# Performance work log

Hardware: AMD Instinct MI355X
Metric: run time of the kernel (lower is better)

Reference implementation:

```python
import jax, jax.numpy as jnp
import numpy as np

B, T, D, H = 2, 2048, 2048, 16
HS = D // H  # head size 128


def setup_inputs() -> dict:
    key = jax.random.key(0)
    ks = jax.random.split(key, 5)
    s = 0.02
    return {
        "x": jax.random.normal(ks[0], (B, T, D), dtype=jnp.float32),
        "wq": jax.random.normal(ks[1], (D, D), dtype=jnp.float32) * s,
        "wk": jax.random.normal(ks[2], (D, D), dtype=jnp.float32) * s,
        "wv": jax.random.normal(ks[3], (D, D), dtype=jnp.float32) * s,
        "wo": jax.random.normal(ks[4], (D, D), dtype=jnp.float32) * s,
    }


def reference(x, wq, wk, wv, wo):
    b, t, d = x.shape
    # projections: nn.Linear(x) = x @ W.T ; here W stored as (out,in)
    q = (x @ wq.T).reshape(b, t, H, HS).transpose(0, 2, 1, 3)  # (B,H,T,HS)
    k = (x @ wk.T).reshape(b, t, H, HS).transpose(0, 2, 1, 3)
    v = (x @ wv.T).reshape(b, t, H, HS).transpose(0, 2, 1, 3)
    scale = 1.0 / np.sqrt(HS).astype(np.float32)
    e = jnp.einsum("bhqd,bhkd->bhqk", q, k) * scale  # (B,H,T,T)
    causal = jnp.tril(jnp.ones((t, t), dtype=bool))
    e = jnp.where(causal[None, None], e, jnp.float32(-jnp.inf))
    alpha = jax.nn.softmax(e, axis=-1)  # dropout=0.0 -> identity
    attn = jnp.einsum("bhqk,bhkd->bhqd", alpha, v)
    attn = attn.transpose(0, 2, 1, 3).reshape(b, t, d)
    return attn @ wo.T
```

## Files before the change

kernel.cpp:

```cpp
#include <hip/hip_runtime.h>
#include <hip/hip_bf16.h>

typedef __bf16 bf16x8 __attribute__((ext_vector_type(8)));
typedef float f32x4 __attribute__((ext_vector_type(4)));
typedef unsigned short u16x8 __attribute__((ext_vector_type(8)));

#define GLDS16(g, s)                                                         \
  __builtin_amdgcn_global_load_lds(                                          \
      (const __attribute__((address_space(1))) void*)(g),                    \
      (__attribute__((address_space(3))) void*)(s), 16, 0, 0)

__device__ __forceinline__ void store1(__hip_bfloat16* p, float v) { *p = __float2bfloat16(v); }
__device__ __forceinline__ void store1(float* p, float v) { *p = v; }

__global__ __launch_bounds__(256) void cast_f32_to_bf16(const float4* __restrict__ in,
                                                        ushort4* __restrict__ out, int n4) {
  int i = blockIdx.x * 256 + threadIdx.x;
  if (i >= n4) return;
  float4 v = in[i];
  union { ushort4 u; __hip_bfloat16 h[4]; } o;
  o.h[0] = __float2bfloat16(v.x);
  o.h[1] = __float2bfloat16(v.y);
  o.h[2] = __float2bfloat16(v.z);
  o.h[3] = __float2bfloat16(v.w);
  out[i] = o.u;
}

template <typename OutT>
__global__ __launch_bounds__(512, 2) void gemm256(const __hip_bfloat16* __restrict__ A,
                                                  const __hip_bfloat16* __restrict__ B0,
                                                  const __hip_bfloat16* __restrict__ B1,
                                                  const __hip_bfloat16* __restrict__ B2,
                                                  OutT* __restrict__ C0,
                                                  OutT* __restrict__ C1,
                                                  OutT* __restrict__ C2,
                                                  int nBx, int nBy, int ntPerMat,
                                                  int N, int K) {
  __shared__ __hip_bfloat16 As[2][256 * 64];
  __shared__ __hip_bfloat16 Bs[2][256 * 64];

  const int t = threadIdx.x;
  const int w = t >> 6, l = t & 63;
  const int lr = l & 15, hi = l >> 4;

  const int nwg = nBx * nBy;
  int id = (int)blockIdx.x;
  id = (id & 7) * (nwg >> 3) + (id >> 3);
  const int bx = id / nBy;
  const int by = id % nBy;

  const int sel = bx / ntPerMat;
  const __hip_bfloat16* Bm = (sel == 0) ? B0 : ((sel == 1) ? B1 : B2);
  OutT* Cm = (sel == 0) ? C0 : ((sel == 1) ? C1 : C2);
  const int n0 = (bx - sel * ntPerMat) * 256;
  const int m0 = by * 256;

  const int c0r = t >> 3, cs = t & 7;
  const int c1r = 64 + c0r;
  const __hip_bfloat16* aP0 = A + (size_t)(m0 + c0r) * K + (cs ^ (c0r & 7)) * 8;
  const __hip_bfloat16* aP1 = A + (size_t)(m0 + c1r) * K + (cs ^ (c1r & 7)) * 8;
  const __hip_bfloat16* bP0 = Bm + (size_t)(n0 + c0r) * K + (cs ^ (c0r & 7)) * 8;
  const __hip_bfloat16* bP1 = Bm + (size_t)(n0 + c1r) * K + (cs ^ (c1r & 7)) * 8;
  const size_t HK = (size_t)128 * K;

#define STAGE_S(sidx, nb, koff)                                              \
  do {                                                                       \
    if ((sidx) == 0) {                                                       \
      GLDS16(aP0 + (koff), (char*)As[nb] + t * 16);                          \
      GLDS16(aP1 + (koff), (char*)As[nb] + 8192 + t * 16);                   \
    } else if ((sidx) == 1) {                                                \
      GLDS16(bP0 + (koff), (char*)Bs[nb] + t * 16);                          \
      GLDS16(bP1 + (koff), (char*)Bs[nb] + 8192 + t * 16);                   \
    } else if ((sidx) == 2) {                                                \
      GLDS16(aP0 + HK + (koff), (char*)As[nb] + 16384 + t * 16);             \
      GLDS16(aP1 + HK + (koff), (char*)As[nb] + 24576 + t * 16);             \
    } else {                                                                 \
      GLDS16(bP0 + HK + (koff), (char*)Bs[nb] + 16384 + t * 16);             \
      GLDS16(bP1 + HK + (koff), (char*)Bs[nb] + 24576 + t * 16);             \
    }                                                                        \
  } while (0)

  f32x4 acc[2][2][4][2] = {};
  bf16x8 af[4][2];
  bf16x8 bqA[2][2], bqB[2][2];
  const int NT = K / 64;
  const int sw = lr & 7;
  const int arow = (w >> 2) * 64;
  const int brow = (w & 3) * 32;

#define LOAD_A(mh)                                                           \
  _Pragma("unroll") for (int mi = 0; mi < 4; ++mi)                           \
    _Pragma("unroll") for (int kk = 0; kk < 2; ++kk)                         \
      af[mi][kk] = *(const bf16x8*)((const char*)As[buf] +                   \
          ((mh) * 128 + arow + mi * 16 + lr) * 128 + (((kk * 4 + hi) ^ sw) << 4));
#define LOAD_B(dst, nh)                                                      \
  _Pragma("unroll") for (int ni = 0; ni < 2; ++ni)                           \
    _Pragma("unroll") for (int kk = 0; kk < 2; ++kk)                         \
      dst[ni][kk] = *(const bf16x8*)((const char*)Bs[buf] +                  \
          ((nh) * 128 + brow + ni * 16 + lr) * 128 + (((kk * 4 + hi) ^ sw) << 4));
#define MFMA_Q(mh, nh, bq)                                                   \
  do {                                                                       \
    __builtin_amdgcn_s_setprio(1);                                           \
    _Pragma("unroll") for (int mi = 0; mi < 4; ++mi)                         \
      _Pragma("unroll") for (int ni = 0; ni < 2; ++ni) {                     \
        acc[mh][nh][mi][ni] = __builtin_amdgcn_mfma_f32_16x16x32_bf16(       \
            af[mi][0], bq[ni][0], acc[mh][nh][mi][ni], 0, 0, 0);             \
        acc[mh][nh][mi][ni] = __builtin_amdgcn_mfma_f32_16x16x32_bf16(       \
            af[mi][1], bq[ni][1], acc[mh][nh][mi][ni], 0, 0, 0);             \
      }                                                                      \
    __builtin_amdgcn_s_setprio(0);                                           \
  } while (0)
#define WAITB(lastt)                                                         \
  do {                                                                       \
    if (lastt) asm volatile("s_waitcnt vmcnt(0)" ::: "memory");              \
    else       asm volatile("s_waitcnt vmcnt(4)" ::: "memory");              \
    __builtin_amdgcn_s_barrier();                                            \
  } while (0)

  STAGE_S(0, 0, 0);
  STAGE_S(1, 0, 0);
  STAGE_S(3, 0, 0);
  STAGE_S(2, 0, 0);

  for (int tt = 0; tt < NT; ++tt) {
    const int buf = tt & 1, nb = buf ^ 1;
    const bool stg = (tt + 1 < NT);
    const bool lastt = !stg;
    const size_t ko = (size_t)(tt + 1) * 64;

    WAITB(lastt);
    LOAD_A(0); LOAD_B(bqA, 0);
    if (stg) STAGE_S(0, nb, ko);
    MFMA_Q(0, 0, bqA);

    WAITB(lastt);
    LOAD_B(bqB, 1);
    if (stg) STAGE_S(1, nb, ko);
    MFMA_Q(0, 1, bqB);

    WAITB(lastt);
    LOAD_A(1);
    if (stg) STAGE_S(3, nb, ko);
    MFMA_Q(1, 1, bqB);

    WAITB(lastt);
    if (stg) STAGE_S(2, nb, ko);
    MFMA_Q(1, 0, bqA);
  }
#undef WAITB
#undef MFMA_Q
#undef LOAD_B
#undef LOAD_A
#undef STAGE_S

#pragma unroll
  for (int mh = 0; mh < 2; ++mh)
#pragma unroll
    for (int nh = 0; nh < 2; ++nh)
#pragma unroll
      for (int mi = 0; mi < 4; ++mi)
#pragma unroll
        for (int ni = 0; ni < 2; ++ni)
#pragma unroll
          for (int i = 0; i < 4; ++i) {
            size_t idx = (size_t)(m0 + mh * 128 + arow + mi * 16 + hi * 4 + i) * N +
                         (n0 + nh * 128 + brow + ni * 16 + lr);
            store1(&Cm[idx], acc[mh][nh][mi][ni][i]);
          }
}

__global__ __launch_bounds__(256, 2) void flash_attn(const __hip_bfloat16* __restrict__ Qg,
                                                     const __hip_bfloat16* __restrict__ Kg,
                                                     const __hip_bfloat16* __restrict__ Vg,
                                                     __hip_bfloat16* __restrict__ Og) {
  __shared__ __hip_bfloat16 Ks[2][64 * 128];
  __shared__ __hip_bfloat16 Vt[128 * 64];

  const int mblk = blockIdx.x;
  const int bh = mblk & 31;
  const int jj = mblk >> 5;
  const int qt = (jj < 8) ? (15 - jj) : (jj - 8);
  const int b = bh >> 4, h = bh & 15;
  const int q0 = qt * 128;
  const int t = threadIdx.x, w = t >> 6, l = t & 63;
  const int lr = l & 15, hi = l >> 4;
  const size_t base = ((size_t)b * 2048) * 2048 + (size_t)h * 128;
  const int nt = 2 * qt + 2;
  const float scale = 0.08838834764831843f;

  const int hi2 = (hi & 1) * 2;
  const int addrA = (((hi2) << 4) | lr) << 2;
  const int addrB = (((hi2 + 1) << 4) | lr) << 2;
  int addr_o[4];
#pragma unroll
  for (int i = 0; i < 4; ++i) addr_o[i] = ((l & 48) | (hi * 4 + i)) << 2;
  const bool hiHigh = (hi >> 1) != 0;

  bf16x8 qf[2][4];
#pragma unroll
  for (int g = 0; g < 2; ++g) {
    const __hip_bfloat16* qrow = Qg + base + (size_t)(q0 + w * 32 + g * 16 + lr) * 2048;
#pragma unroll
    for (int kk = 0; kk < 4; ++kk)
      qf[g][kk] = *(const bf16x8*)(qrow + kk * 32 + hi * 8);
  }

  f32x4 o_acc[2][8] = {};
  float m_run[2] = {-1e30f, -1e30f};
  float l_run[2] = {0.f, 0.f};

  const __hip_bfloat16* kptr[4];
#pragma unroll
  for (int i = 0; i < 4; ++i) {
    int c = i * 256 + t;
    int kr = c >> 4;
    int ke = ((c & 15) ^ (kr & 7)) * 8;
    kptr[i] = Kg + base + (size_t)kr * 2048 + ke;
  }
  const __hip_bfloat16* vptr[2];
#pragma unroll
  for (int it = 0; it < 2; ++it) {
    int kp = it * 16 + w * 4 + hi;
    vptr[it] = Vg + base + (size_t)(kp * 2) * 2048 + lr * 8;
  }

  u16x8 va[2], vb[2];
#pragma unroll
  for (int i = 0; i < 4; ++i)
    GLDS16(kptr[i], (char*)Ks[0] + (i * 256 + t) * 16);
#pragma unroll
  for (int it = 0; it < 2; ++it) {
    va[it] = *(const u16x8*)vptr[it];
    vb[it] = *(const u16x8*)(vptr[it] + 2048);
  }

  for (int kt = 0; kt < nt; ++kt) {
    const int cur = kt & 1;
    const int kb = kt * 64;
    __syncthreads();

#pragma unroll
    for (int it = 0; it < 2; ++it)
#pragma unroll
      for (int j2 = 0; j2 < 8; ++j2) {
        int d = lr * 8 + j2;
        int sw = (lr ^ j2) & 7;
        int off = d * 128 + (((it * 4 + w) ^ sw) << 4) + hi * 4;
        *(unsigned int*)((char*)Vt + off) =
            (unsigned int)va[it][j2] | ((unsigned int)vb[it][j2] << 16);
      }
    if (kt + 1 < nt) {
      const size_t adv = (size_t)(kb + 64) * 2048;
#pragma unroll
      for (int i = 0; i < 4; ++i)
        GLDS16(kptr[i] + adv, (char*)Ks[cur ^ 1] + (i * 256 + t) * 16);
#pragma unroll
      for (int it = 0; it < 2; ++it) {
        va[it] = *(const u16x8*)(vptr[it] + adv);
        vb[it] = *(const u16x8*)(vptr[it] + adv + 2048);
      }
    }
    asm volatile("s_waitcnt lgkmcnt(0)" ::: "memory");
    __builtin_amdgcn_s_barrier();

    if (!(kt == nt - 1 && w < 2)) {
      const char* ks = (const char*)Ks[cur];

      f32x4 st[2][4];
#pragma unroll
      for (int g = 0; g < 2; ++g)
#pragma unroll
        for (int nk = 0; nk < 4; ++nk) { f32x4 z = {}; st[g][nk] = z; }
#pragma unroll
      for (int nk = 0; nk < 4; ++nk)
#pragma unroll
        for (int kk = 0; kk < 4; ++kk) {
          bf16x8 kf = *(const bf16x8*)(ks + (nk * 16 + lr) * 256 +
                                       (((kk * 4 + hi) ^ (lr & 7)) << 4));
#pragma unroll
          for (int g = 0; g < 2; ++g)
            st[g][nk] = __builtin_amdgcn_mfma_f32_16x16x32_bf16(kf, qf[g][kk], st[g][nk], 0, 0, 0);
        }

      const bool maskt = (kt >= nt - 2);
#pragma unroll
      for (int g = 0; g < 2; ++g)
#pragma unroll
        for (int nk = 0; nk < 4; ++nk)
#pragma unroll
          for (int i = 0; i < 4; ++i) {
            float v = st[g][nk][i] * scale;
            if (maskt) {
              int ki = kb + nk * 16 + hi * 4 + i;
              int qi = q0 + w * 32 + g * 16 + lr;
              if (ki > qi) v = -1e30f;
            }
            st[g][nk][i] = v;
          }

      bf16x8 paf[2][2];
#pragma unroll
      for (int g = 0; g < 2; ++g) {
        float t0 = fmaxf(fmaxf(st[g][0][0], st[g][0][1]), fmaxf(st[g][0][2], st[g][0][3]));
        float t1 = fmaxf(fmaxf(st[g][1][0], st[g][1][1]), fmaxf(st[g][1][2], st[g][1][3]));
        float t2 = fmaxf(fmaxf(st[g][2][0], st[g][2][1]), fmaxf(st[g][2][2], st[g][2][3]));
        float t3 = fmaxf(fmaxf(st[g][3][0], st[g][3][1]), fmaxf(st[g][3][2], st[g][3][3]));
        float mx = fmaxf(fmaxf(t0, t1), fmaxf(t2, t3));
        mx = fmaxf(mx, __shfl_xor(mx, 16));
        mx = fmaxf(mx, __shfl_xor(mx, 32));

        if (!__all(mx - m_run[g] <= 8.0f)) {
          float mnew = fmaxf(m_run[g], mx);
          float rs = __expf(m_run[g] - mnew);
          m_run[g] = mnew;
          l_run[g] *= rs;
          int rsi = __float_as_int(rs);
#pragma unroll
          for (int i = 0; i < 4; ++i) {
            float rso = __int_as_float(__builtin_amdgcn_ds_bpermute(addr_o[i], rsi));
#pragma unroll
            for (int nc = 0; nc < 8; ++nc) o_acc[g][nc][i] *= rso;
          }
        }

#pragma unroll
        for (int nk = 0; nk < 4; ++nk)
#pragma unroll
          for (int i = 0; i < 4; ++i)
            st[g][nk][i] = __expf(st[g][nk][i] - m_run[g]);

        float s0 = (st[g][0][0] + st[g][0][1]) + (st[g][0][2] + st[g][0][3]);
        float s1 = (st[g][1][0] + st[g][1][1]) + (st[g][1][2] + st[g][1][3]);
        float s2 = (st[g][2][0] + st[g][2][1]) + (st[g][2][2] + st[g][2][3]);
        float s3 = (st[g][3][0] + st[g][3][1]) + (st[g][3][2] + st[g][3][3]);
        float sm = (s0 + s1) + (s2 + s3);
        sm += __shfl_xor(sm, 16);
        sm += __shfl_xor(sm, 32);
        l_run[g] += sm;

        unsigned pk[4][2];
#pragma unroll
        for (int nk = 0; nk < 4; ++nk) {
          asm("v_cvt_pk_bf16_f32 %0, %1, %2"
              : "=v"(pk[nk][0]) : "v"(st[g][nk][0]), "v"(st[g][nk][1]));
          asm("v_cvt_pk_bf16_f32 %0, %1, %2"
              : "=v"(pk[nk][1]) : "v"(st[g][nk][2]), "v"(st[g][nk][3]));
        }

#pragma unroll
        for (int kk = 0; kk < 2; ++kk) {
          unsigned au[4];
#pragma unroll
          for (int p = 0; p < 4; ++p) {
            int ad = (p < 2) ? addrA : addrB;
            int v0 = __builtin_amdgcn_ds_bpermute(ad, (int)pk[2 * kk][p & 1]);
            int v1 = __builtin_amdgcn_ds_bpermute(ad, (int)pk[2 * kk + 1][p & 1]);
            au[p] = hiHigh ? (unsigned)v1 : (unsigned)v0;
          }
          union { unsigned u[4]; bf16x8 v; } cv;
          cv.u[0] = au[0]; cv.u[1] = au[1]; cv.u[2] = au[2]; cv.u[3] = au[3];
          paf[g][kk] = cv.v;
        }
      }

#pragma unroll
      for (int kk = 0; kk < 2; ++kk)
#pragma unroll
        for (int nc = 0; nc < 8; ++nc) {
          int d = nc * 16 + lr;
          int sw = ((d >> 3) ^ d) & 7;
          bf16x8 vfr = *(const bf16x8*)((const char*)Vt + d * 128 +
                                        (((kk * 4 + hi) ^ sw) << 4));
#pragma unroll
          for (int g = 0; g < 2; ++g)
            o_acc[g][nc] = __builtin_amdgcn_mfma_f32_16x16x32_bf16(paf[g][kk], vfr, o_acc[g][nc], 0, 0, 0);
        }
    }
  }

#pragma unroll
  for (int g = 0; g < 2; ++g) {
    float lo[4];
#pragma unroll
    for (int i = 0; i < 4; ++i)
      lo[i] = __int_as_float(__builtin_amdgcn_ds_bpermute(addr_o[i], __float_as_int(l_run[g])));
#pragma unroll
    for (int nc = 0; nc < 8; ++nc)
#pragma unroll
      for (int i = 0; i < 4; ++i) {
        float val = o_acc[g][nc][i] / lo[i];
        Og[base + (size_t)(q0 + w * 32 + g * 16 + hi * 4 + i) * 2048 + nc * 16 + lr] =
            __float2bfloat16(val);
      }
  }
}

extern "C" void kernel_launch(void* const* d_in, const int* in_sizes, int n_in,
                              void* d_out, int out_size, void* d_ws, size_t ws_size,
                              hipStream_t stream) {
  const float* x  = (const float*)d_in[0];
  const float* wq = (const float*)d_in[1];
  const float* wk = (const float*)d_in[2];
  const float* wv = (const float*)d_in[3];
  const float* wo = (const float*)d_in[4];
  float* out = (float*)d_out;

  const int BT = 4096, D = 2048;
  const size_t ND = (size_t)D * D;
  const size_t NX = (size_t)BT * D;

  __hip_bfloat16* xb  = (__hip_bfloat16*)d_ws;
  __hip_bfloat16* wqb = xb + NX;
  __hip_bfloat16* wkb = wqb + ND;
  __hip_bfloat16* wvb = wkb + ND;
  __hip_bfloat16* wob = wvb + ND;
  __hip_bfloat16* Qb  = wob + ND;
  __hip_bfloat16* Kb  = Qb + NX;
  __hip_bfloat16* Vb  = Kb + NX;
  __hip_bfloat16* Ab  = Vb + NX;

  cast_f32_to_bf16<<<(int)(NX / 4 / 256), 256, 0, stream>>>((const float4*)x,  (ushort4*)xb,  (int)(NX / 4));
  cast_f32_to_bf16<<<(int)(ND / 4 / 256), 256, 0, stream>>>((const float4*)wq, (ushort4*)wqb, (int)(ND / 4));
  cast_f32_to_bf16<<<(int)(ND / 4 / 256), 256, 0, stream>>>((const float4*)wk, (ushort4*)wkb, (int)(ND / 4));
  cast_f32_to_bf16<<<(int)(ND / 4 / 256), 256, 0, stream>>>((const float4*)wv, (ushort4*)wvb, (int)(ND / 4));
  cast_f32_to_bf16<<<(int)(ND / 4 / 256), 256, 0, stream>>>((const float4*)wo, (ushort4*)wob, (int)(ND / 4));

  gemm256<__hip_bfloat16><<<384, 512, 0, stream>>>(xb, wqb, wkb, wvb, Qb, Kb, Vb,
                                                   24, 16, 8, D, D);

  flash_attn<<<512, 256, 0, stream>>>(Qb, Kb, Vb, Ab);

  gemm256<float><<<128, 512, 0, stream>>>(Ab, wob, wob, wob, out, out, out,
                                          8, 16, 8, D, D);
}
```

Measured before the change: 291.8 us.

## Split-K output projection with atomics, software-pipeline LDS reads, fuse weight casts

The output projection GEMM now splits K in two across 256 workgroups and accumulates into a zeroed fp32 output with atomicAdd. Before, it ran only 128 workgroups, which underfills the GPU. The GEMM main loop now double-buffers A fragments and prefetches the next tile's first fragments from LDS before the loop boundary, with relaxed vmcnt waits. This lets LDS reads overlap the MFMAs. The four weight casts are fused into a single launch. The cost is an extra memset, atomic traffic on the output, and a summation order that is no longer deterministic.

New measurement: 329.4 us. 1.13x slower.

```diff
diff --git a/kernel.cpp b/kernel.cpp
--- a/kernel.cpp
+++ b/kernel.cpp
@@ -26,7 +26,29 @@
   out[i] = o.u;
 }
 
-template <typename OutT>
+__global__ __launch_bounds__(256) void cast4_f32_to_bf16(const float4* __restrict__ w0,
+                                                         const float4* __restrict__ w1,
+                                                         const float4* __restrict__ w2,
+                                                         const float4* __restrict__ w3,
+                                                         ushort4* __restrict__ o0,
+                                                         ushort4* __restrict__ o1,
+                                                         ushort4* __restrict__ o2,
+                                                         ushort4* __restrict__ o3, int n4) {
+  int i = blockIdx.x * 256 + threadIdx.x;
+  if (i >= n4) return;
+  int s = blockIdx.y;
+  const float4* in = (s == 0) ? w0 : (s == 1) ? w1 : (s == 2) ? w2 : w3;
+  ushort4* out = (s == 0) ? o0 : (s == 1) ? o1 : (s == 2) ? o2 : o3;
+  float4 v = in[i];
+  union { ushort4 u; __hip_bfloat16 h[4]; } o;
+  o.h[0] = __float2bfloat16(v.x);
+  o.h[1] = __float2bfloat16(v.y);
+  o.h[2] = __float2bfloat16(v.z);
+  o.h[3] = __float2bfloat16(v.w);
+  out[i] = o.u;
+}
+
+template <typename OutT, bool ATOMIC, bool KSPLIT>
 __global__ __launch_bounds__(512, 2) void gemm256(const __hip_bfloat16* __restrict__ A,
                                                   const __hip_bfloat16* __restrict__ B0,
                                                   const __hip_bfloat16* __restrict__ B1,
@@ -43,8 +65,14 @@
   const int w = t >> 6, l = t & 63;
   const int lr = l & 15, hi = l >> 4;
 
+  int id = (int)blockIdx.x;
+  int k0 = 0, Klen = K;
+  if (KSPLIT) {
+    k0 = (id >> 7) * (K >> 1);
+    Klen = K >> 1;
+    id &= 127;
+  }
   const int nwg = nBx * nBy;
-  int id = (int)blockIdx.x;
   id = (id & 7) * (nwg >> 3) + (id >> 3);
   const int bx = id / nBy;
   const int by = id % nBy;
@@ -57,10 +85,10 @@
 
   const int c0r = t >> 3, cs = t & 7;
   const int c1r = 64 + c0r;
-  const __hip_bfloat16* aP0 = A + (size_t)(m0 + c0r) * K + (cs ^ (c0r & 7)) * 8;
-  const __hip_bfloat16* aP1 = A + (size_t)(m0 + c1r) * K + (cs ^ (c1r & 7)) * 8;
-  const __hip_bfloat16* bP0 = Bm + (size_t)(n0 + c0r) * K + (cs ^ (c0r & 7)) * 8;
-  const __hip_bfloat16* bP1 = Bm + (size_t)(n0 + c1r) * K + (cs ^ (c1r & 7)) * 8;
+  const __hip_bfloat16* aP0 = A + (size_t)(m0 + c0r) * K + k0 + (cs ^ (c0r & 7)) * 8;
+  const __hip_bfloat16* aP1 = A + (size_t)(m0 + c1r) * K + k0 + (cs ^ (c1r & 7)) * 8;
+  const __hip_bfloat16* bP0 = Bm + (size_t)(n0 + c0r) * K + k0 + (cs ^ (c0r & 7)) * 8;
+  const __hip_bfloat16* bP1 = Bm + (size_t)(n0 + c1r) * K + k0 + (cs ^ (c1r & 7)) * 8;
   const size_t HK = (size_t)128 * K;
 
 #define STAGE_S(sidx, nb, koff)                                              \
@@ -81,46 +109,45 @@
   } while (0)
 
   f32x4 acc[2][2][4][2] = {};
-  bf16x8 af[4][2];
+  bf16x8 afA[4][2], afB[4][2];
   bf16x8 bqA[2][2], bqB[2][2];
-  const int NT = K / 64;
+  const int NT = Klen / 64;
   const int sw = lr & 7;
   const int arow = (w >> 2) * 64;
   const int brow = (w & 3) * 32;
 
-#define LOAD_A(mh)                                                           \
+#define RD_A(dst, mh, bufid)                                                 \
   _Pragma("unroll") for (int mi = 0; mi < 4; ++mi)                           \
     _Pragma("unroll") for (int kk = 0; kk < 2; ++kk)                         \
-      af[mi][kk] = *(const bf16x8*)((const char*)As[buf] +                   \
+      dst[mi][kk] = *(const bf16x8*)((const char*)As[bufid] +                \
           ((mh) * 128 + arow + mi * 16 + lr) * 128 + (((kk * 4 + hi) ^ sw) << 4));
-#define LOAD_B(dst, nh)                                                      \
+#define RD_B(dst, nh, bufid)                                                 \
   _Pragma("unroll") for (int ni = 0; ni < 2; ++ni)                           \
     _Pragma("unroll") for (int kk = 0; kk < 2; ++kk)                         \
-      dst[ni][kk] = *(const bf16x8*)((const char*)Bs[buf] +                  \
+      dst[ni][kk] = *(const bf16x8*)((const char*)Bs[bufid] +                \
           ((nh) * 128 + brow + ni * 16 + lr) * 128 + (((kk * 4 + hi) ^ sw) << 4));
-#define MFMA_Q(mh, nh, bq)                                                   \
+#define MFMA_Q(mh, nh, afv, bq)                                              \
   do {                                                                       \
     __builtin_amdgcn_s_setprio(1);                                           \
     _Pragma("unroll") for (int mi = 0; mi < 4; ++mi)                         \
       _Pragma("unroll") for (int ni = 0; ni < 2; ++ni) {                     \
         acc[mh][nh][mi][ni] = __builtin_amdgcn_mfma_f32_16x16x32_bf16(       \
-            af[mi][0], bq[ni][0], acc[mh][nh][mi][ni], 0, 0, 0);             \
+            afv[mi][0], bq[ni][0], acc[mh][nh][mi][ni], 0, 0, 0);            \
         acc[mh][nh][mi][ni] = __builtin_amdgcn_mfma_f32_16x16x32_bf16(       \
-            af[mi][1], bq[ni][1], acc[mh][nh][mi][ni], 0, 0, 0);             \
+            afv[mi][1], bq[ni][1], acc[mh][nh][mi][ni], 0, 0, 0);            \
       }                                                                      \
     __builtin_amdgcn_s_setprio(0);                                           \
   } while (0)
-#define WAITB(lastt)                                                         \
-  do {                                                                       \
-    if (lastt) asm volatile("s_waitcnt vmcnt(0)" ::: "memory");              \
-    else       asm volatile("s_waitcnt vmcnt(4)" ::: "memory");              \
-    __builtin_amdgcn_s_barrier();                                            \
-  } while (0)
+#define WAITV(n)  asm volatile("s_waitcnt vmcnt(" #n ")" ::: "memory")
 
   STAGE_S(0, 0, 0);
   STAGE_S(1, 0, 0);
   STAGE_S(3, 0, 0);
   STAGE_S(2, 0, 0);
+  WAITV(4);
+  __builtin_amdgcn_s_barrier();
+  RD_A(afA, 0, 0);
+  RD_B(bqA, 0, 0);
 
   for (int tt = 0; tt < NT; ++tt) {
     const int buf = tt & 1, nb = buf ^ 1;
@@ -128,29 +155,36 @@
     const bool lastt = !stg;
     const size_t ko = (size_t)(tt + 1) * 64;
 
-    WAITB(lastt);
-    LOAD_A(0); LOAD_B(bqA, 0);
+    if (lastt) WAITV(0); else WAITV(2);
+    __builtin_amdgcn_s_barrier();
+    MFMA_Q(0, 0, afA, bqA);
+    RD_B(bqB, 1, buf);
     if (stg) STAGE_S(0, nb, ko);
-    MFMA_Q(0, 0, bqA);
-
-    WAITB(lastt);
-    LOAD_B(bqB, 1);
+
+    if (lastt) WAITV(0); else WAITV(2);
+    __builtin_amdgcn_s_barrier();
+    MFMA_Q(0, 1, afA, bqB);
+    RD_A(afB, 1, buf);
     if (stg) STAGE_S(1, nb, ko);
-    MFMA_Q(0, 1, bqB);
-
-    WAITB(lastt);
-    LOAD_A(1);
+
+    if (lastt) WAITV(0);
+    __builtin_amdgcn_s_barrier();
+    MFMA_Q(1, 1, afB, bqB);
     if (stg) STAGE_S(3, nb, ko);
-    MFMA_Q(1, 1, bqB);
-
-    WAITB(lastt);
-    if (stg) STAGE_S(2, nb, ko);
-    MFMA_Q(1, 0, bqA);
-  }
-#undef WAITB
+
+    if (lastt) WAITV(0); else WAITV(2);
+    __builtin_amdgcn_s_barrier();
+    MFMA_Q(1, 0, afB, bqA);
+    if (stg) {
+      RD_A(afA, 0, nb);
+      RD_B(bqA, 0, nb);
+      STAGE_S(2, nb, ko);
+    }
+  }
+#undef WAITV
 #undef MFMA_Q
-#undef LOAD_B
-#undef LOAD_A
+#undef RD_B
+#undef RD_A
 #undef STAGE_S
 
 #pragma unroll
@@ -165,7 +199,10 @@
           for (int i = 0; i < 4; ++i) {
             size_t idx = (size_t)(m0 + mh * 128 + arow + mi * 16 + hi * 4 + i) * N +
                          (n0 + nh * 128 + brow + ni * 16 + lr);
-            store1(&Cm[idx], acc[mh][nh][mi][ni][i]);
+            if (ATOMIC)
+              atomicAdd((float*)&Cm[idx], acc[mh][nh][mi][ni][i]);
+            else
+              store1(&Cm[idx], acc[mh][nh][mi][ni][i]);
           }
 }
 
@@ -419,17 +456,18 @@
   __hip_bfloat16* Vb  = Kb + NX;
   __hip_bfloat16* Ab  = Vb + NX;
 
-  cast_f32_to_bf16<<<(int)(NX / 4 / 256), 256, 0, stream>>>((const float4*)x,  (ushort4*)xb,  (int)(NX / 4));
-  cast_f32_to_bf16<<<(int)(ND / 4 / 256), 256, 0, stream>>>((const float4*)wq, (ushort4*)wqb, (int)(ND / 4));
-  cast_f32_to_bf16<<<(int)(ND / 4 / 256), 256, 0, stream>>>((const float4*)wk, (ushort4*)wkb, (int)(ND / 4));
-  cast_f32_to_bf16<<<(int)(ND / 4 / 256), 256, 0, stream>>>((const float4*)wv, (ushort4*)wvb, (int)(ND / 4));
-  cast_f32_to_bf16<<<(int)(ND / 4 / 256), 256, 0, stream>>>((const float4*)wo, (ushort4*)wob, (int)(ND / 4));
-
-  gemm256<__hip_bfloat16><<<384, 512, 0, stream>>>(xb, wqb, wkb, wvb, Qb, Kb, Vb,
-                                                   24, 16, 8, D, D);
+  hipMemsetAsync(out, 0, (size_t)BT * D * sizeof(float), stream);
+
+  cast_f32_to_bf16<<<(int)(NX / 4 / 256), 256, 0, stream>>>((const float4*)x, (ushort4*)xb, (int)(NX / 4));
+  cast4_f32_to_bf16<<<dim3((int)(ND / 4 / 256), 4), 256, 0, stream>>>(
+      (const float4*)wq, (const float4*)wk, (const float4*)wv, (const float4*)wo,
+      (ushort4*)wqb, (ushort4*)wkb, (ushort4*)wvb, (ushort4*)wob, (int)(ND / 4));
+
+  gemm256<__hip_bfloat16, false, false><<<384, 512, 0, stream>>>(
+      xb, wqb, wkb, wvb, Qb, Kb, Vb, 24, 16, 8, D, D);
 
   flash_attn<<<512, 256, 0, stream>>>(Qb, Kb, Vb, Ab);
 
-  gemm256<float><<<128, 512, 0, stream>>>(Ab, wob, wob, wob, out, out, out,
-                                          8, 16, 8, D, D);
+  gemm256<float, true, true><<<256, 512, 0, stream>>>(
+      Ab, wob, wob, wob, out, out, out, 8, 16, 8, D, D);
 }
```
